# Kernel optimization log

Hardware: AMD Instinct MI355X
Metric: run time of the kernel (lower is better)

Reference implementation:

```python
import jax, jax.numpy as jnp
import numpy as np

IN_DIM = 2
OUT_DIM = 3  # number of independent CScalar heads (u, v, p)
HID = 16
N = 4194304


def setup_inputs() -> dict:
    key = jax.random.key(0)
    ks = jax.random.split(key, 7)
    s1 = 1.0 / np.sqrt(IN_DIM)
    s2 = 1.0 / np.sqrt(HID)
    x = jax.random.normal(ks[0], (N, IN_DIM), dtype=jnp.float32)
    # Stacked parameters for the OUT_DIM independent tiny MLPs
    W1 = jax.random.uniform(ks[1], (OUT_DIM, IN_DIM, HID), jnp.float32, -s1, s1)
    b1 = jax.random.uniform(ks[2], (OUT_DIM, HID), jnp.float32, -s1, s1)
    W2 = jax.random.uniform(ks[3], (OUT_DIM, HID, HID), jnp.float32, -s2, s2)
    b2 = jax.random.uniform(ks[4], (OUT_DIM, HID), jnp.float32, -s2, s2)
    W3 = jax.random.uniform(ks[5], (OUT_DIM, HID), jnp.float32, -s2, s2)  # last layer HID->1, squeezed
    b3 = jax.random.uniform(ks[6], (OUT_DIM,), jnp.float32, -s2, s2)
    return {"x": x, "W1": W1, "b1": b1, "W2": W2, "b2": b2, "W3": W3, "b3": b3}


def reference(x, W1, b1, W2, b2, W3, b3):
    # All OUT_DIM tiny MLPs batched as one grouped GEMM chain.
    # h1: [E, N, H]
    h1 = jax.nn.relu(jnp.einsum('ni,eih->enh', x, W1) + b1[:, None, :])
    h2 = jax.nn.relu(jnp.einsum('enh,ehk->enk', h1, W2) + b2[:, None, :])
    y = jnp.einsum('enh,eh->en', h2, W3) + b3[:, None]  # [E, N]
    return y.T  # [N, E] == torch.hstack of per-head [N,1] outputs
```

## Files before the change

kernel.cpp:

```cpp
#include <hip/hip_runtime.h>
#include <hip/hip_bf16.h>

typedef __attribute__((ext_vector_type(2)))  float f32x2;
typedef __attribute__((ext_vector_type(4)))  float f32x4;
typedef __attribute__((ext_vector_type(8)))  float f32x8;
typedef __attribute__((ext_vector_type(16))) float f32x16;
typedef __attribute__((ext_vector_type(2)))  __bf16 bf16x2;
typedef __attribute__((ext_vector_type(8)))  __bf16 bf16x8;
typedef __attribute__((ext_vector_type(4)))  unsigned int u32x4;
typedef __attribute__((ext_vector_type(2)))  int i32x2;

static __device__ __forceinline__ bf16x8 cvt8(f32x8 v) {
    return __builtin_convertvector(v, bf16x8);
}
static __device__ __forceinline__ unsigned int pk2(float a, float b) {
    f32x2 v = {a, b};
    return __builtin_bit_cast(unsigned int, __builtin_convertvector(v, bf16x2));
}

#define MFMA32(A, B, C) __builtin_amdgcn_mfma_f32_32x32x16_bf16((A), (B), (C), 0, 0, 0)

static __device__ __forceinline__ bf16x8 pack_frag(
    float d0, float d1, float d2, float d3,
    float d4, float d5, float d6, float d7) {
    unsigned int q0 = pk2(d0, d1), q1 = pk2(d2, d3);
    unsigned int q2 = pk2(d4, d5), q3 = pk2(d6, d7);
    i32x2 s02 = __builtin_amdgcn_permlane32_swap((int)q0, (int)q2, false, false);
    i32x2 s13 = __builtin_amdgcn_permlane32_swap((int)q1, (int)q3, false, false);
    u32x4 u = { (unsigned)s02[0], (unsigned)s13[0], (unsigned)s02[1], (unsigned)s13[1] };
    return __builtin_bit_cast(bf16x8, u);
}

__global__ __launch_bounds__(256, 3) void mlp3_mfma32(
    const float* __restrict__ x,
    const float* __restrict__ W1, const float* __restrict__ b1,
    const float* __restrict__ W2, const float* __restrict__ b2,
    const float* __restrict__ W3, const float* __restrict__ b3,
    float* __restrict__ out, int n)
{
    const int tid  = (int)threadIdx.x;
    const int lane = tid & 63;
    const int row  = lane & 31;
    const int h    = lane >> 5;
    const int wv   = tid >> 6;

    bf16x8 a1[3], a2[3], a3[3];
    f32x4 b2lo[3], b2hi[3];
    #pragma unroll
    for (int e = 0; e < 3; ++e) {
        f32x8 t = {0.f,0.f,0.f,0.f,0.f,0.f,0.f,0.f};
        if (h == 0 && row < 16) {
            t[0] = W1[e * 32 + row];
            t[1] = W1[e * 32 + 16 + row];
            t[2] = b1[e * 16 + row];
        }
        a1[e] = cvt8(t);
        f32x8 t2 = {0.f,0.f,0.f,0.f,0.f,0.f,0.f,0.f};
        if (row < 16) {
            #pragma unroll
            for (int i = 0; i < 8; ++i)
                t2[i] = W2[e * 256 + (8 * h + i) * 16 + row];
        }
        a2[e] = cvt8(t2);
        f32x8 t3 = {0.f,0.f,0.f,0.f,0.f,0.f,0.f,0.f};
        if (row == e) {
            #pragma unroll
            for (int i = 0; i < 8; ++i)
                t3[i] = W3[e * 16 + 8 * h + i];
        }
        a3[e] = cvt8(t3);
        #pragma unroll
        for (int r = 0; r < 4; ++r) {
            b2lo[e][r] = b2[e * 16 + (r & 3) + 4 * h];
            b2hi[e][r] = b2[e * 16 + (r & 3) + 8 + 4 * h];
        }
    }
    const float b30 = b3[0], b31 = b3[1], b32 = b3[2];
    f32x16 zz;
    #pragma unroll
    for (int r = 0; r < 16; ++r) zz[r] = 0.f;

    const int xoff = (wv * 32 + row) * 8;
    const int ooff = (wv * 32 + row) * 12;

    const int nblk   = n >> 7;
    const int stride = (int)gridDim.x;

    int cb = (int)blockIdx.x;
    float2 xv = *reinterpret_cast<const float2*>(
        (const char*)x + (size_t)cb * 1024 + xoff);

    while (true) {
        const int nb = cb + stride;
        const bool more = nb < nblk;
        float2 xn;
        if (more)
            xn = *reinterpret_cast<const float2*>(
                (const char*)x + (size_t)nb * 1024 + xoff);

        u32x4 bxu = { pk2(xv.x, xv.y), 0x3F80u, 0u, 0u };
        const bf16x8 bx = __builtin_bit_cast(bf16x8, bxu);

        f32x16 y = zz;
        #pragma unroll
        for (int e = 0; e < 3; ++e) {
            f32x16 t1 = MFMA32(a1[e], bx, zz);
            bf16x8 bh = pack_frag(
                fmaxf(t1[0], 0.f), fmaxf(t1[1], 0.f), fmaxf(t1[2], 0.f), fmaxf(t1[3], 0.f),
                fmaxf(t1[4], 0.f), fmaxf(t1[5], 0.f), fmaxf(t1[6], 0.f), fmaxf(t1[7], 0.f));
            f32x16 t2 = MFMA32(a2[e], bh, zz);
            bf16x8 bt = pack_frag(
                fmaxf(t2[0] + b2lo[e][0], 0.f), fmaxf(t2[1] + b2lo[e][1], 0.f),
                fmaxf(t2[2] + b2lo[e][2], 0.f), fmaxf(t2[3] + b2lo[e][3], 0.f),
                fmaxf(t2[4] + b2hi[e][0], 0.f), fmaxf(t2[5] + b2hi[e][1], 0.f),
                fmaxf(t2[6] + b2hi[e][2], 0.f), fmaxf(t2[7] + b2hi[e][3], 0.f));
            y = MFMA32(a3[e], bt, y);
        }

        if (lane < 32) {
            float3 o = make_float3(y[0] + b30, y[1] + b31, y[2] + b32);
            *reinterpret_cast<float3*>(
                (char*)out + (size_t)cb * 1536 + ooff) = o;
        }

        if (!more) break;
        cb = nb;
        xv = xn;
    }
}

extern "C" void kernel_launch(void* const* d_in, const int* in_sizes, int n_in,
                              void* d_out, int out_size, void* d_ws, size_t ws_size,
                              hipStream_t stream) {
    const float* x  = (const float*)d_in[0];
    const float* W1 = (const float*)d_in[1];
    const float* b1 = (const float*)d_in[2];
    const float* W2 = (const float*)d_in[3];
    const float* b2 = (const float*)d_in[4];
    const float* W3 = (const float*)d_in[5];
    const float* b3 = (const float*)d_in[6];
    float* out = (float*)d_out;
    (void)d_ws; (void)ws_size; (void)n_in; (void)out_size;

    const int n = in_sizes[0] / 2;
    const int block = 256;
    const int grid = 2048;

    mlp3_mfma32<<<grid, block, 0, stream>>>(x, W1, b1, W2, b2, W3, b3, out, n);
}
```

Before: 55.75 us.

## Process two MFMA tiles per wave and remove permlane swaps via reordered weight k-index

Each wave now handles two independent 32-row tiles per iteration, so a block covers 256 rows and the two MFMA dependency chains interleave to hide latency. The k-dimension of W2/W3 is permuted at load time to match the MFMA accumulator output layout, which removes the permlane32_swap shuffles when packing the ReLU output into the next B operand. The costs are more registers (two accumulator sets) and a grid that covers half as many blocks per sweep.

```diff
diff --git a/kernel.cpp b/kernel.cpp
--- a/kernel.cpp
+++ b/kernel.cpp
@@ -8,7 +8,6 @@
 typedef __attribute__((ext_vector_type(2)))  __bf16 bf16x2;
 typedef __attribute__((ext_vector_type(8)))  __bf16 bf16x8;
 typedef __attribute__((ext_vector_type(4)))  unsigned int u32x4;
-typedef __attribute__((ext_vector_type(2)))  int i32x2;
 
 static __device__ __forceinline__ bf16x8 cvt8(f32x8 v) {
     return __builtin_convertvector(v, bf16x8);
@@ -20,14 +19,19 @@
 
 #define MFMA32(A, B, C) __builtin_amdgcn_mfma_f32_32x32x16_bf16((A), (B), (C), 0, 0, 0)
 
-static __device__ __forceinline__ bf16x8 pack_frag(
-    float d0, float d1, float d2, float d3,
-    float d4, float d5, float d6, float d7) {
-    unsigned int q0 = pk2(d0, d1), q1 = pk2(d2, d3);
-    unsigned int q2 = pk2(d4, d5), q3 = pk2(d6, d7);
-    i32x2 s02 = __builtin_amdgcn_permlane32_swap((int)q0, (int)q2, false, false);
-    i32x2 s13 = __builtin_amdgcn_permlane32_swap((int)q1, (int)q3, false, false);
-    u32x4 u = { (unsigned)s02[0], (unsigned)s13[0], (unsigned)s02[1], (unsigned)s13[1] };
+static __device__ __forceinline__ bf16x8 relu_pack(const f32x16& t) {
+    u32x4 u = { pk2(fmaxf(t[0], 0.f), fmaxf(t[1], 0.f)),
+                pk2(fmaxf(t[2], 0.f), fmaxf(t[3], 0.f)),
+                pk2(fmaxf(t[4], 0.f), fmaxf(t[5], 0.f)),
+                pk2(fmaxf(t[6], 0.f), fmaxf(t[7], 0.f)) };
+    return __builtin_bit_cast(bf16x8, u);
+}
+static __device__ __forceinline__ bf16x8 relu_pack_b2(const f32x16& t,
+                                                      const f32x4& lo, const f32x4& hi) {
+    u32x4 u = { pk2(fmaxf(t[0] + lo[0], 0.f), fmaxf(t[1] + lo[1], 0.f)),
+                pk2(fmaxf(t[2] + lo[2], 0.f), fmaxf(t[3] + lo[3], 0.f)),
+                pk2(fmaxf(t[4] + hi[0], 0.f), fmaxf(t[5] + hi[1], 0.f)),
+                pk2(fmaxf(t[6] + hi[2], 0.f), fmaxf(t[7] + hi[3], 0.f)) };
     return __builtin_bit_cast(bf16x8, u);
 }
 
@@ -58,21 +62,25 @@
         f32x8 t2 = {0.f,0.f,0.f,0.f,0.f,0.f,0.f,0.f};
         if (row < 16) {
             #pragma unroll
-            for (int i = 0; i < 8; ++i)
-                t2[i] = W2[e * 256 + (8 * h + i) * 16 + row];
+            for (int i = 0; i < 8; ++i) {
+                const int k = (i & 3) + 8 * (i >> 2) + 4 * h;
+                t2[i] = W2[e * 256 + k * 16 + row];
+            }
         }
         a2[e] = cvt8(t2);
         f32x8 t3 = {0.f,0.f,0.f,0.f,0.f,0.f,0.f,0.f};
         if (row == e) {
             #pragma unroll
-            for (int i = 0; i < 8; ++i)
-                t3[i] = W3[e * 16 + 8 * h + i];
+            for (int i = 0; i < 8; ++i) {
+                const int k = (i & 3) + 8 * (i >> 2) + 4 * h;
+                t3[i] = W3[e * 16 + k];
+            }
         }
         a3[e] = cvt8(t3);
         #pragma unroll
         for (int r = 0; r < 4; ++r) {
-            b2lo[e][r] = b2[e * 16 + (r & 3) + 4 * h];
-            b2hi[e][r] = b2[e * 16 + (r & 3) + 8 + 4 * h];
+            b2lo[e][r] = b2[e * 16 + r + 4 * h];
+            b2hi[e][r] = b2[e * 16 + r + 8 + 4 * h];
         }
     }
     const float b30 = b3[0], b31 = b3[1], b32 = b3[2];
@@ -80,52 +88,61 @@
     #pragma unroll
     for (int r = 0; r < 16; ++r) zz[r] = 0.f;
 
-    const int xoff = (wv * 32 + row) * 8;
-    const int ooff = (wv * 32 + row) * 12;
+    const int xoff = (wv * 64 + row) * 8;
+    const int ooff = (wv * 64 + row) * 12;
 
-    const int nblk   = n >> 7;
+    const int nblk   = n >> 8;
     const int stride = (int)gridDim.x;
 
     int cb = (int)blockIdx.x;
-    float2 xv = *reinterpret_cast<const float2*>(
-        (const char*)x + (size_t)cb * 1024 + xoff);
+    float2 xv0 = *reinterpret_cast<const float2*>((const char*)x + (size_t)cb * 2048 + xoff);
+    float2 xv1 = *reinterpret_cast<const float2*>((const char*)x + (size_t)cb * 2048 + xoff + 256);
 
     while (true) {
         const int nb = cb + stride;
         const bool more = nb < nblk;
-        float2 xn;
-        if (more)
-            xn = *reinterpret_cast<const float2*>(
-                (const char*)x + (size_t)nb * 1024 + xoff);
+        float2 xn0, xn1;
+        if (more) {
+            xn0 = *reinterpret_cast<const float2*>((const char*)x + (size_t)nb * 2048 + xoff);
+            xn1 = *reinterpret_cast<const float2*>((const char*)x + (size_t)nb * 2048 + xoff + 256);
+        }
 
-        u32x4 bxu = { pk2(xv.x, xv.y), 0x3F80u, 0u, 0u };
-        const bf16x8 bx = __builtin_bit_cast(bf16x8, bxu);
+        u32x4 bu0 = { pk2(xv0.x, xv0.y), 0x3F80u, 0u, 0u };
+        u32x4 bu1 = { pk2(xv1.x, xv1.y), 0x3F80u, 0u, 0u };
+        const bf16x8 bx0 = __builtin_bit_cast(bf16x8, bu0);
+        const bf16x8 bx1 = __builtin_bit_cast(bf16x8, bu1);
 
-        f32x16 y = zz;
+        f32x16 y0, y1;
         #pragma unroll
         for (int e = 0; e < 3; ++e) {
-            f32x16 t1 = MFMA32(a1[e], bx, zz);
-            bf16x8 bh = pack_frag(
-                fmaxf(t1[0], 0.f), fmaxf(t1[1], 0.f), fmaxf(t1[2], 0.f), fmaxf(t1[3], 0.f),
-                fmaxf(t1[4], 0.f), fmaxf(t1[5], 0.f), fmaxf(t1[6], 0.f), fmaxf(t1[7], 0.f));
-            f32x16 t2 = MFMA32(a2[e], bh, zz);
-            bf16x8 bt = pack_frag(
-                fmaxf(t2[0] + b2lo[e][0], 0.f), fmaxf(t2[1] + b2lo[e][1], 0.f),
-                fmaxf(t2[2] + b2lo[e][2], 0.f), fmaxf(t2[3] + b2lo[e][3], 0.f),
-                fmaxf(t2[4] + b2hi[e][0], 0.f), fmaxf(t2[5] + b2hi[e][1], 0.f),
-                fmaxf(t2[6] + b2hi[e][2], 0.f), fmaxf(t2[7] + b2hi[e][3], 0.f));
-            y = MFMA32(a3[e], bt, y);
+            f32x16 t10 = MFMA32(a1[e], bx0, zz);
+            f32x16 t11 = MFMA32(a1[e], bx1, zz);
+            bf16x8 bh0 = relu_pack(t10);
+            bf16x8 bh1 = relu_pack(t11);
+            f32x16 t20 = MFMA32(a2[e], bh0, zz);
+            f32x16 t21 = MFMA32(a2[e], bh1, zz);
+            bf16x8 bt0 = relu_pack_b2(t20, b2lo[e], b2hi[e]);
+            bf16x8 bt1 = relu_pack_b2(t21, b2lo[e], b2hi[e]);
+            if (e == 0) {
+                y0 = MFMA32(a3[0], bt0, zz);
+                y1 = MFMA32(a3[0], bt1, zz);
+            } else {
+                y0 = MFMA32(a3[e], bt0, y0);
+                y1 = MFMA32(a3[e], bt1, y1);
+            }
         }
 
         if (lane < 32) {
-            float3 o = make_float3(y[0] + b30, y[1] + b31, y[2] + b32);
-            *reinterpret_cast<float3*>(
-                (char*)out + (size_t)cb * 1536 + ooff) = o;
+            char* ob = (char*)out + (size_t)cb * 3072 + ooff;
+            *reinterpret_cast<float3*>(ob) =
+                make_float3(y0[0] + b30, y0[1] + b31, y0[2] + b32);
+            *reinterpret_cast<float3*>(ob + 384) =
+                make_float3(y1[0] + b30, y1[1] + b31, y1[2] + b32);
         }
 
         if (!more) break;
         cb = nb;
-        xv = xn;
+        xv0 = xn0; xv1 = xn1;
     }
 }
 
```

Measured after the change: 49.83 us. -10.6%, faster.

## Replace permlane swaps and final MFMA with register-layout remap and packed dot

Applied to the files above, without the earlier changes.

The W2 A-fragment rows are permuted so the first-layer MFMA output can feed the second MFMA directly, removing the permlane32 swaps between layers. The last HID->1 layer no longer uses an MFMA: each lane does a packed-fp32 multiply-add over its accumulator values against W3 and combines halves with one cross-lane shuffle. This cuts MFMA count and cross-lane traffic per tile, in exchange for a shuffle and extra VALU work. The last layer now runs in fp32 instead of bf16, which slightly changes numerics.

```diff
diff --git a/kernel.cpp b/kernel.cpp
--- a/kernel.cpp
+++ b/kernel.cpp
@@ -2,34 +2,24 @@
 #include <hip/hip_bf16.h>
 
 typedef __attribute__((ext_vector_type(2)))  float f32x2;
-typedef __attribute__((ext_vector_type(4)))  float f32x4;
 typedef __attribute__((ext_vector_type(8)))  float f32x8;
 typedef __attribute__((ext_vector_type(16))) float f32x16;
 typedef __attribute__((ext_vector_type(2)))  __bf16 bf16x2;
 typedef __attribute__((ext_vector_type(8)))  __bf16 bf16x8;
 typedef __attribute__((ext_vector_type(4)))  unsigned int u32x4;
-typedef __attribute__((ext_vector_type(2)))  int i32x2;
 
 static __device__ __forceinline__ bf16x8 cvt8(f32x8 v) {
     return __builtin_convertvector(v, bf16x8);
 }
-static __device__ __forceinline__ unsigned int pk2(float a, float b) {
-    f32x2 v = {a, b};
+static __device__ __forceinline__ unsigned int pkcvt(f32x2 v) {
     return __builtin_bit_cast(unsigned int, __builtin_convertvector(v, bf16x2));
+}
+static __device__ __forceinline__ f32x2 max2(f32x2 v) {
+    const f32x2 z = {0.f, 0.f};
+    return __builtin_elementwise_max(v, z);
 }
 
 #define MFMA32(A, B, C) __builtin_amdgcn_mfma_f32_32x32x16_bf16((A), (B), (C), 0, 0, 0)
-
-static __device__ __forceinline__ bf16x8 pack_frag(
-    float d0, float d1, float d2, float d3,
-    float d4, float d5, float d6, float d7) {
-    unsigned int q0 = pk2(d0, d1), q1 = pk2(d2, d3);
-    unsigned int q2 = pk2(d4, d5), q3 = pk2(d6, d7);
-    i32x2 s02 = __builtin_amdgcn_permlane32_swap((int)q0, (int)q2, false, false);
-    i32x2 s13 = __builtin_amdgcn_permlane32_swap((int)q1, (int)q3, false, false);
-    u32x4 u = { (unsigned)s02[0], (unsigned)s13[0], (unsigned)s02[1], (unsigned)s13[1] };
-    return __builtin_bit_cast(bf16x8, u);
-}
 
 __global__ __launch_bounds__(256, 3) void mlp3_mfma32(
     const float* __restrict__ x,
@@ -44,8 +34,8 @@
     const int h    = lane >> 5;
     const int wv   = tid >> 6;
 
-    bf16x8 a1[3], a2[3], a3[3];
-    f32x4 b2lo[3], b2hi[3];
+    bf16x8 a1[3], a2[3];
+    f32x2  w3p[3][4], b2p[3][4];
     #pragma unroll
     for (int e = 0; e < 3; ++e) {
         f32x8 t = {0.f,0.f,0.f,0.f,0.f,0.f,0.f,0.f};
@@ -58,21 +48,19 @@
         f32x8 t2 = {0.f,0.f,0.f,0.f,0.f,0.f,0.f,0.f};
         if (row < 16) {
             #pragma unroll
-            for (int i = 0; i < 8; ++i)
-                t2[i] = W2[e * 256 + (8 * h + i) * 16 + row];
+            for (int i = 0; i < 8; ++i) {
+                const int k = (i & 3) + 8 * (i >> 2) + 4 * h;
+                t2[i] = W2[e * 256 + k * 16 + row];
+            }
         }
         a2[e] = cvt8(t2);
-        f32x8 t3 = {0.f,0.f,0.f,0.f,0.f,0.f,0.f,0.f};
-        if (row == e) {
-            #pragma unroll
-            for (int i = 0; i < 8; ++i)
-                t3[i] = W3[e * 16 + 8 * h + i];
-        }
-        a3[e] = cvt8(t3);
         #pragma unroll
-        for (int r = 0; r < 4; ++r) {
-            b2lo[e][r] = b2[e * 16 + (r & 3) + 4 * h];
-            b2hi[e][r] = b2[e * 16 + (r & 3) + 8 + 4 * h];
+        for (int j = 0; j < 4; ++j) {
+            const int i0 = 2 * j, i1 = 2 * j + 1;
+            const int k0 = (i0 & 3) + 8 * (i0 >> 2) + 4 * h;
+            const int k1 = (i1 & 3) + 8 * (i1 >> 2) + 4 * h;
+            w3p[e][j] = (f32x2){ W3[e * 16 + k0], W3[e * 16 + k1] };
+            b2p[e][j] = (f32x2){ b2[e * 16 + k0], b2[e * 16 + k1] };
         }
     }
     const float b30 = b3[0], b31 = b3[1], b32 = b3[2];
@@ -87,40 +75,42 @@
     const int stride = (int)gridDim.x;
 
     int cb = (int)blockIdx.x;
-    float2 xv = *reinterpret_cast<const float2*>(
-        (const char*)x + (size_t)cb * 1024 + xoff);
+    float2 xv = *reinterpret_cast<const float2*>((const char*)x + (size_t)cb * 1024 + xoff);
 
     while (true) {
         const int nb = cb + stride;
         const bool more = nb < nblk;
         float2 xn;
         if (more)
-            xn = *reinterpret_cast<const float2*>(
-                (const char*)x + (size_t)nb * 1024 + xoff);
+            xn = *reinterpret_cast<const float2*>((const char*)x + (size_t)nb * 1024 + xoff);
 
-        u32x4 bxu = { pk2(xv.x, xv.y), 0x3F80u, 0u, 0u };
-        const bf16x8 bx = __builtin_bit_cast(bf16x8, bxu);
+        u32x4 bu = { pkcvt((f32x2){xv.x, xv.y}), 0x3F80u, 0u, 0u };
+        const bf16x8 bx = __builtin_bit_cast(bf16x8, bu);
 
-        f32x16 y = zz;
+        float ys[3];
         #pragma unroll
         for (int e = 0; e < 3; ++e) {
             f32x16 t1 = MFMA32(a1[e], bx, zz);
-            bf16x8 bh = pack_frag(
-                fmaxf(t1[0], 0.f), fmaxf(t1[1], 0.f), fmaxf(t1[2], 0.f), fmaxf(t1[3], 0.f),
-                fmaxf(t1[4], 0.f), fmaxf(t1[5], 0.f), fmaxf(t1[6], 0.f), fmaxf(t1[7], 0.f));
+            u32x4 bhw;
+            #pragma unroll
+            for (int j = 0; j < 4; ++j)
+                bhw[j] = pkcvt(max2((f32x2){ t1[2*j], t1[2*j+1] }));
+            const bf16x8 bh = __builtin_bit_cast(bf16x8, bhw);
+
             f32x16 t2 = MFMA32(a2[e], bh, zz);
-            bf16x8 bt = pack_frag(
-                fmaxf(t2[0] + b2lo[e][0], 0.f), fmaxf(t2[1] + b2lo[e][1], 0.f),
-                fmaxf(t2[2] + b2lo[e][2], 0.f), fmaxf(t2[3] + b2lo[e][3], 0.f),
-                fmaxf(t2[4] + b2hi[e][0], 0.f), fmaxf(t2[5] + b2hi[e][1], 0.f),
-                fmaxf(t2[6] + b2hi[e][2], 0.f), fmaxf(t2[7] + b2hi[e][3], 0.f));
-            y = MFMA32(a3[e], bt, y);
+            f32x2 yp = {0.f, 0.f};
+            #pragma unroll
+            for (int j = 0; j < 4; ++j) {
+                f32x2 q = max2((f32x2){ t2[2*j], t2[2*j+1] } + b2p[e][j]);
+                yp += w3p[e][j] * q;
+            }
+            const float ysum = yp[0] + yp[1];
+            ys[e] = ysum + __shfl_xor(ysum, 32, 64);
         }
 
         if (lane < 32) {
-            float3 o = make_float3(y[0] + b30, y[1] + b31, y[2] + b32);
-            *reinterpret_cast<float3*>(
-                (char*)out + (size_t)cb * 1536 + ooff) = o;
+            *reinterpret_cast<float3*>((char*)out + (size_t)cb * 1536 + ooff) =
+                make_float3(ys[0] + b30, ys[1] + b31, ys[2] + b32);
         }
 
         if (!more) break;
```

Measured after the change: 51.44 us. 1.08x faster.
